# Performance work log

Measured on AMD Instinct MI355X. Metric: run time of the kernel, lower is better.

Reference implementation:

```python
import jax, jax.numpy as jnp
import numpy as np

B, L, F, H, N_HASHES = 2, 2048, 1024, 16, 4
HD = F // H  # head_dim = 64


def setup_inputs() -> dict:
    key = jax.random.key(0)
    ks = jax.random.split(key, 8)
    s = 0.02
    return {
        "x": jax.random.normal(ks[0], (B, L, F), jnp.float32),
        "Wqk": jax.random.normal(ks[1], (F, 2 * F), jnp.float32) * s,
        "bqk": jnp.zeros((2 * F,), jnp.float32),
        "Wv": jax.random.normal(ks[2], (F, F), jnp.float32) * s,
        "bv": jnp.zeros((F,), jnp.float32),
        "Wo": jax.random.normal(ks[3], (F, F), jnp.float32) * s,
        "bo": jnp.zeros((F,), jnp.float32),
        "R": jax.random.normal(ks[4], (H, N_HASHES, HD), jnp.float32) * s,
    }


def reference(x, Wqk, bqk, Wv, bv, Wo, bo, R):
    b, l, f = x.shape
    h, _, hd = R.shape

    qk = x @ Wqk + bqk                      # [B,L,2F]
    q, k = jnp.split(qk, 2, axis=-1)
    v = x @ Wv + bv                         # [B,L,F]

    def to_heads(t):
        return t.reshape(b, l, h, hd).transpose(0, 2, 1, 3)  # [B,H,L,D]

    q, k, v = to_heads(q), to_heads(k), to_heads(v)

    # LSH hashing of queries: argmax over [rotated, -rotated]
    rotated = jnp.einsum('bhld,hrd->bhlr', q, R)             # [B,H,L,n_hashes]
    buckets = jnp.argmax(jnp.concatenate([rotated, -rotated], axis=-1), axis=-1)  # [B,H,L]

    # Sort sequence positions by bucket id (per batch/head)
    idx = jnp.argsort(buckets, axis=-1)                      # [B,H,L]

    def gather_l(t):
        return jnp.take_along_axis(t, idx[..., None], axis=2)

    sq, sk, sv = gather_l(q), gather_l(k), gather_l(v)

    # Full dense attention over the sorted sequence
    scale = 1.0 / np.sqrt(hd).astype(np.float32)
    dots = jnp.einsum('bhqd,bhkd->bhqk', sq, sk) * scale     # [B,H,L,L]
    attn = jax.nn.softmax(dots, axis=-1)
    out = jnp.einsum('bhqk,bhkd->bhqd', attn, sv)            # [B,H,L,D]

    # Scatter back to original order
    restore = jnp.argsort(idx, axis=-1)
    out = jnp.take_along_axis(out, restore[..., None], axis=2)
    out = out.transpose(0, 2, 1, 3).reshape(b, l, f)
    return out @ Wo + bo
```

## Files before the change

kernel.cpp:

```cpp
#include <hip/hip_runtime.h>


#define B_ 2
#define L_ 2048
#define F_ 1024
#define H_ 16
#define D_ 64
#define M_ 4096

typedef unsigned short u16;
typedef unsigned int   u32;
typedef __bf16 bf16x8 __attribute__((ext_vector_type(8)));
typedef float  f32x4  __attribute__((ext_vector_type(4)));

__device__ __forceinline__ u16 f2bf(float f) {
    __bf16 h = (__bf16)f;
    return __builtin_bit_cast(u16, h);
}

__device__ __forceinline__ void glds16(const void* g, void* l) {
    __builtin_amdgcn_global_load_lds(
        (const __attribute__((address_space(1))) u32*)g,
        (__attribute__((address_space(3))) u32*)l, 16, 0, 0);
}

#define MFMA16(a, b, c) __builtin_amdgcn_mfma_f32_16x16x32_bf16(a, b, c, 0, 0, 0)

__global__ __launch_bounds__(256) void cast_x(const float* __restrict__ x, u16* __restrict__ xb) {
    int i0 = blockIdx.x * 256 + threadIdx.x;
    #pragma unroll
    for (int r = 0; r < 4; ++r) {
        int i = i0 + r * 262144;
        float4 v = ((const float4*)x)[i];
        ushort4 o; o.x = f2bf(v.x); o.y = f2bf(v.y); o.z = f2bf(v.z); o.w = f2bf(v.w);
        ((ushort4*)xb)[i] = o;
    }
}

__global__ __launch_bounds__(256) void tr_all(
    const float* __restrict__ Wqk, const float* __restrict__ Wv,
    const float* __restrict__ Wo, u16* __restrict__ Wt, u16* __restrict__ Wot)
{
    __shared__ float tile[32][33];
    const int z = blockIdx.z;
    const float* src; u16* dst; int N;
    if (z == 0)      { src = Wqk; dst = Wt;                       N = 2048; }
    else if (z == 1) { src = Wv;  dst = Wt + (size_t)2048 * 1024; N = 1024; }
    else             { src = Wo;  dst = Wot;                      N = 1024; }
    int n0 = blockIdx.x * 32, k0 = blockIdx.y * 32;
    if (n0 >= N) return;
    int tx = threadIdx.x & 31, ty = threadIdx.x >> 5;
    #pragma unroll
    for (int i = 0; i < 4; ++i) {
        int k = ty + i * 8;
        tile[k][tx] = src[(size_t)(k0 + k) * N + n0 + tx];
    }
    __syncthreads();
    #pragma unroll
    for (int i = 0; i < 4; ++i) {
        int n = ty + i * 8;
        dst[(size_t)(n0 + n) * 1024 + k0 + tx] = f2bf(tile[tx][n]);
    }
}

__device__ __forceinline__ void gemm_loop(
    const u16* __restrict__ A, const u16* __restrict__ Bt,
    size_t m0, size_t n0, u16* As, u16* Bs, int t, f32x4 acc[4][4])
{
    const int w = t >> 6, lane = t & 63, ml = lane & 15, quad = lane >> 4;
    const int mw = (w >> 1) * 64, nw = (w & 1) * 64;
    const int srow = (lane >> 2), schunk = (lane & 3) * 8;

    for (int k0 = 0; k0 < 1024; k0 += 32) {
        __syncthreads();
        #pragma unroll
        for (int i = 0; i < 2; ++i) {
            int row = w * 32 + i * 16 + srow;
            glds16(A  + (m0 + row) * 1024 + k0 + schunk, As + (w * 32 + i * 16) * 32);
            glds16(Bt + (n0 + row) * 1024 + k0 + schunk, Bs + (w * 32 + i * 16) * 32);
        }
        __syncthreads();
        bf16x8 af[4], bf_[4];
        #pragma unroll
        for (int mt = 0; mt < 4; ++mt)
            af[mt] = *(const bf16x8*)(As + (mw + mt * 16 + ml) * 32 + quad * 8);
        #pragma unroll
        for (int nt = 0; nt < 4; ++nt)
            bf_[nt] = *(const bf16x8*)(Bs + (nw + nt * 16 + ml) * 32 + quad * 8);
        #pragma unroll
        for (int mt = 0; mt < 4; ++mt)
            #pragma unroll
            for (int nt = 0; nt < 4; ++nt)
                acc[mt][nt] = MFMA16(af[mt], bf_[nt], acc[mt][nt]);
    }
}

__global__ __launch_bounds__(256) void qkv_gemm(
    const u16* __restrict__ xb, const u16* __restrict__ Wt,
    const float* __restrict__ bqk, const float* __restrict__ bv,
    u16* __restrict__ Qb, u16* __restrict__ Kb, u16* __restrict__ Vt)
{
    __shared__ __align__(16) u16 As[128 * 32];
    __shared__ __align__(16) u16 Bs[128 * 32];
    const int t = threadIdx.x;
    const size_t m0 = blockIdx.y * 128, n0 = blockIdx.x * 128;
    f32x4 acc[4][4] = {};
    gemm_loop(xb, Wt, m0, n0, As, Bs, t, acc);

    const int w = t >> 6, lane = t & 63, ml = lane & 15, quad = lane >> 4;
    const int mw = (w >> 1) * 64, nw = (w & 1) * 64;
    const int seg = (int)(n0 >> 10);

    #pragma unroll
    for (int mt = 0; mt < 4; ++mt) {
        #pragma unroll
        for (int nt = 0; nt < 4; ++nt) {
            f32x4 a = acc[mt][nt];
            int c = (int)n0 + nw + nt * 16 + ml;
            int mbase = (int)m0 + mw + mt * 16 + quad * 4;
            if (seg == 2) {
                int cv = c - 2048, h = cv >> 6, d = cv & 63;
                float bias = bv[cv];
                int bb = mbase >> 11, l0 = mbase & (L_ - 1);
                ushort4 pk;
                pk.x = f2bf(a[0] + bias); pk.y = f2bf(a[1] + bias);
                pk.z = f2bf(a[2] + bias); pk.w = f2bf(a[3] + bias);
                *(ushort4*)&Vt[(((size_t)(bb * H_ + h)) * D_ + d) * L_ + l0] = pk;
            } else {
                float bias = bqk[c];
                float sc = (seg == 0) ? 0.125f : 1.0f;
                u16* dst = (seg == 0) ? Qb : Kb;
                int cc = c & 1023, h = cc >> 6, d = cc & 63;
                #pragma unroll
                for (int reg = 0; reg < 4; ++reg) {
                    int m = mbase + reg, bb = m >> 11, l = m & (L_ - 1);
                    dst[(((size_t)(bb * H_ + h)) * L_ + l) * D_ + d] = f2bf((a[reg] + bias) * sc);
                }
            }
        }
    }
}

__global__ __launch_bounds__(256) void out_gemm(
    const u16* __restrict__ Ob, const u16* __restrict__ Wot,
    const float* __restrict__ bo, float* __restrict__ out)
{
    __shared__ __align__(16) u16 As[128 * 32];
    __shared__ __align__(16) u16 Bs[128 * 32];
    const int t = threadIdx.x;
    const size_t m0 = blockIdx.y * 128, n0 = blockIdx.x * 128;
    f32x4 acc[4][4] = {};
    gemm_loop(Ob, Wot, m0, n0, As, Bs, t, acc);

    const int w = t >> 6, lane = t & 63, ml = lane & 15, quad = lane >> 4;
    const int mw = (w >> 1) * 64, nw = (w & 1) * 64;
    #pragma unroll
    for (int mt = 0; mt < 4; ++mt)
        #pragma unroll
        for (int nt = 0; nt < 4; ++nt) {
            int c = (int)n0 + nw + nt * 16 + ml;
            int mbase = (int)m0 + mw + mt * 16 + quad * 4;
            float bias = bo[c];
            #pragma unroll
            for (int reg = 0; reg < 4; ++reg)
                out[(size_t)(mbase + reg) * F_ + c] = acc[mt][nt][reg] + bias;
        }
}

__device__ __forceinline__ bf16x8 frag(const u16* base, int row, int chunk) {
    return *(const bf16x8*)(base + row * 64 + ((chunk ^ (row & 7)) << 3));
}

__global__ __launch_bounds__(256) void attn_mfma(
    const u16* __restrict__ Qb, const u16* __restrict__ Kb,
    const u16* __restrict__ Vt, u16* __restrict__ Ob)
{
    __shared__ __align__(16) u16 Qs[128 * 64];
    __shared__ __align__(16) u16 Ks[64 * 64];
    __shared__ __align__(16) u16 Vs[64 * 64];
    __shared__ __align__(16) float Sw[4][32 * 68];
    __shared__ float Ls[4][32];

    const int t = threadIdx.x, w = t >> 6, lane = t & 63;
    const int ml = lane & 15, quad = lane >> 4;
    const int srow8 = lane >> 3, sch = lane & 7;
    const int qt = blockIdx.x, h = blockIdx.y, b = blockIdx.z;
    const size_t hoff = ((size_t)(b * H_ + h)) * L_ * D_;
    const u16* Qg = Qb + hoff + (size_t)qt * 128 * 64;
    const u16* Kg = Kb + hoff;
    const u16* Vg = Vt + hoff;

    #pragma unroll
    for (int i = 0; i < 4; ++i) {
        int row = w * 32 + i * 8 + srow8;
        int ch = sch ^ (row & 7);
        glds16(Qg + row * 64 + ch * 8, Qs + (w * 32 + i * 8) * 64);
    }
    __syncthreads();
    bf16x8 aq[2][2];
    #pragma unroll
    for (int m2 = 0; m2 < 2; ++m2)
        #pragma unroll
        for (int k2 = 0; k2 < 2; ++k2)
            aq[m2][k2] = frag(Qs, w * 32 + m2 * 16 + ml, k2 * 4 + quad);

    float psum[2] = {0.f, 0.f};
    f32x4 oacc[2][4] = {};
    float* Swp = Sw[w];

    for (int kt = 0; kt < 32; ++kt) {
        __syncthreads();
        #pragma unroll
        for (int i = 0; i < 2; ++i) {
            int row = w * 16 + i * 8 + srow8;
            int ch = sch ^ (row & 7);
            glds16(Kg + (size_t)(kt * 64 + row) * 64 + ch * 8, Ks + (w * 16 + i * 8) * 64);
            glds16(Vg + (size_t)row * L_ + kt * 64 + ch * 8,   Vs + (w * 16 + i * 8) * 64);
        }
        __syncthreads();

        f32x4 sacc[2][4] = {};
        #pragma unroll
        for (int k2 = 0; k2 < 2; ++k2) {
            bf16x8 bk[4];
            #pragma unroll
            for (int nt = 0; nt < 4; ++nt)
                bk[nt] = frag(Ks, nt * 16 + ml, k2 * 4 + quad);
            #pragma unroll
            for (int m2 = 0; m2 < 2; ++m2)
                #pragma unroll
                for (int nt = 0; nt < 4; ++nt)
                    sacc[m2][nt] = MFMA16(aq[m2][k2], bk[nt], sacc[m2][nt]);
        }

        #pragma unroll
        for (int m2 = 0; m2 < 2; ++m2)
            #pragma unroll
            for (int nt = 0; nt < 4; ++nt)
                #pragma unroll
                for (int r = 0; r < 4; ++r) {
                    int row = m2 * 16 + quad * 4 + r, col = nt * 16 + ml;
                    Swp[row * 68 + col] = __expf(sacc[m2][nt][r]);
                }

        #pragma unroll
        for (int k2 = 0; k2 < 2; ++k2) {
            bf16x8 bv8[4];
            #pragma unroll
            for (int nt = 0; nt < 4; ++nt)
                bv8[nt] = frag(Vs, nt * 16 + ml, k2 * 4 + quad);
            #pragma unroll
            for (int m2 = 0; m2 < 2; ++m2) {
                const float* pp = Swp + (m2 * 16 + ml) * 68 + (k2 * 4 + quad) * 8;
                f32x4 p0 = *(const f32x4*)pp;
                f32x4 p1 = *(const f32x4*)(pp + 4);
                psum[m2] += (p0[0] + p0[1] + p0[2] + p0[3]) +
                            (p1[0] + p1[1] + p1[2] + p1[3]);
                bf16x8 ap;
                ap[0] = (__bf16)p0[0]; ap[1] = (__bf16)p0[1];
                ap[2] = (__bf16)p0[2]; ap[3] = (__bf16)p0[3];
                ap[4] = (__bf16)p1[0]; ap[5] = (__bf16)p1[1];
                ap[6] = (__bf16)p1[2]; ap[7] = (__bf16)p1[3];
                #pragma unroll
                for (int nt = 0; nt < 4; ++nt)
                    oacc[m2][nt] = MFMA16(ap, bv8[nt], oacc[m2][nt]);
            }
        }
    }

    #pragma unroll
    for (int m2 = 0; m2 < 2; ++m2) {
        psum[m2] += __shfl_xor(psum[m2], 16);
        psum[m2] += __shfl_xor(psum[m2], 32);
    }
    if (quad == 0) { Ls[w][ml] = psum[0]; Ls[w][16 + ml] = psum[1]; }

    #pragma unroll
    for (int m2 = 0; m2 < 2; ++m2)
        #pragma unroll
        for (int r = 0; r < 4; ++r) {
            float il = 1.0f / Ls[w][m2 * 16 + quad * 4 + r];
            int row = b * L_ + qt * 128 + w * 32 + m2 * 16 + quad * 4 + r;
            #pragma unroll
            for (int nt = 0; nt < 4; ++nt) {
                int c = h * 64 + nt * 16 + ml;
                Ob[(size_t)row * F_ + c] = f2bf(oacc[m2][nt][r] * il);
            }
        }
}

extern "C" void kernel_launch(void* const* d_in, const int* in_sizes, int n_in,
                              void* d_out, int out_size, void* d_ws, size_t ws_size,
                              hipStream_t stream)
{
    const float* x   = (const float*)d_in[0];
    const float* Wqk = (const float*)d_in[1];
    const float* bqk = (const float*)d_in[2];
    const float* Wv  = (const float*)d_in[3];
    const float* bv  = (const float*)d_in[4];
    const float* Wo  = (const float*)d_in[5];
    const float* bo  = (const float*)d_in[6];
    (void)in_sizes; (void)n_in; (void)out_size; (void)ws_size;
    float* out = (float*)d_out;

    u16* w16 = (u16*)d_ws;
    u16* xb  = w16;
    u16* Wt  = xb  + 4194304;
    u16* Wot = Wt  + 3145728;
    u16* Qb  = Wot + 1048576;
    u16* Kb  = Qb  + 4194304;
    u16* Vtw = Kb  + 4194304;
    u16* Ob  = Vtw + 4194304;

    cast_x<<<1024, 256, 0, stream>>>(x, xb);
    tr_all<<<dim3(64, 32, 3), 256, 0, stream>>>(Wqk, Wv, Wo, Wt, Wot);
    qkv_gemm<<<dim3(24, 32), 256, 0, stream>>>(xb, Wt, bqk, bv, Qb, Kb, Vtw);
    attn_mfma<<<dim3(16, 16, 2), 256, 0, stream>>>(Qb, Kb, Vtw, Ob);
    out_gemm<<<dim3(8, 32), 256, 0, stream>>>(Ob, Wot, bo, out);
}
```

Before: 219.3 us.

## Drop LDS staging in attention; compute transposed scores in registers

The attention kernel stops staging Q, K and V tiles and exp-scores in shared memory. Each wave now loads its MFMA fragments straight from global memory and computes S^T (K as the A operand), so the exp'd probabilities already sit in the register layout needed for the P·V MFMA. This removes the LDS round-trip and all block-level barriers. The cost is that each wave re-reads K and V from global/L2 on its own, with narrow 8-byte loads for V, and the launch is flattened to 1D with a 2-blocks-per-CU occupancy hint.

```diff
diff --git a/kernel.cpp b/kernel.cpp
--- a/kernel.cpp
+++ b/kernel.cpp
@@ -167,105 +167,74 @@
         }
 }
 
-__device__ __forceinline__ bf16x8 frag(const u16* base, int row, int chunk) {
-    return *(const bf16x8*)(base + row * 64 + ((chunk ^ (row & 7)) << 3));
-}
-
-__global__ __launch_bounds__(256) void attn_mfma(
+__global__ __launch_bounds__(256, 2) void attn_mfma(
     const u16* __restrict__ Qb, const u16* __restrict__ Kb,
     const u16* __restrict__ Vt, u16* __restrict__ Ob)
 {
-    __shared__ __align__(16) u16 Qs[128 * 64];
-    __shared__ __align__(16) u16 Ks[64 * 64];
-    __shared__ __align__(16) u16 Vs[64 * 64];
-    __shared__ __align__(16) float Sw[4][32 * 68];
-    __shared__ float Ls[4][32];
-
     const int t = threadIdx.x, w = t >> 6, lane = t & 63;
     const int ml = lane & 15, quad = lane >> 4;
-    const int srow8 = lane >> 3, sch = lane & 7;
-    const int qt = blockIdx.x, h = blockIdx.y, b = blockIdx.z;
+    const int blk = blockIdx.x;
+    const int qt4 = blk & 15, bh = blk >> 4;
+    const int b = bh >> 4, h = bh & 15;
+    const int qbase = qt4 * 128 + w * 32;
     const size_t hoff = ((size_t)(b * H_ + h)) * L_ * D_;
-    const u16* Qg = Qb + hoff + (size_t)qt * 128 * 64;
+    const u16* Qg = Qb + hoff;
     const u16* Kg = Kb + hoff;
     const u16* Vg = Vt + hoff;
 
-    #pragma unroll
-    for (int i = 0; i < 4; ++i) {
-        int row = w * 32 + i * 8 + srow8;
-        int ch = sch ^ (row & 7);
-        glds16(Qg + row * 64 + ch * 8, Qs + (w * 32 + i * 8) * 64);
-    }
-    __syncthreads();
-    bf16x8 aq[2][2];
+    bf16x8 qf[2][2];
     #pragma unroll
     for (int m2 = 0; m2 < 2; ++m2)
         #pragma unroll
         for (int k2 = 0; k2 < 2; ++k2)
-            aq[m2][k2] = frag(Qs, w * 32 + m2 * 16 + ml, k2 * 4 + quad);
-
+            qf[m2][k2] = *(const bf16x8*)(Qg + (size_t)(qbase + m2 * 16 + ml) * 64 + k2 * 32 + quad * 8);
+
+    f32x4 oacc[2][4] = {};
     float psum[2] = {0.f, 0.f};
-    f32x4 oacc[2][4] = {};
-    float* Swp = Sw[w];
 
     for (int kt = 0; kt < 32; ++kt) {
-        __syncthreads();
-        #pragma unroll
-        for (int i = 0; i < 2; ++i) {
-            int row = w * 16 + i * 8 + srow8;
-            int ch = sch ^ (row & 7);
-            glds16(Kg + (size_t)(kt * 64 + row) * 64 + ch * 8, Ks + (w * 16 + i * 8) * 64);
-            glds16(Vg + (size_t)row * L_ + kt * 64 + ch * 8,   Vs + (w * 16 + i * 8) * 64);
-        }
-        __syncthreads();
+        const u16* Kt = Kg + (size_t)kt * 64 * 64;
+
+        bf16x8 kf[4][2];
+        #pragma unroll
+        for (int t4 = 0; t4 < 4; ++t4)
+            #pragma unroll
+            for (int k2 = 0; k2 < 2; ++k2)
+                kf[t4][k2] = *(const bf16x8*)(Kt + (size_t)(t4 * 16 + ml) * 64 + k2 * 32 + quad * 8);
 
         f32x4 sacc[2][4] = {};
         #pragma unroll
-        for (int k2 = 0; k2 < 2; ++k2) {
-            bf16x8 bk[4];
-            #pragma unroll
-            for (int nt = 0; nt < 4; ++nt)
-                bk[nt] = frag(Ks, nt * 16 + ml, k2 * 4 + quad);
-            #pragma unroll
-            for (int m2 = 0; m2 < 2; ++m2)
-                #pragma unroll
-                for (int nt = 0; nt < 4; ++nt)
-                    sacc[m2][nt] = MFMA16(aq[m2][k2], bk[nt], sacc[m2][nt]);
-        }
-
+        for (int k2 = 0; k2 < 2; ++k2)
+            #pragma unroll
+            for (int t4 = 0; t4 < 4; ++t4)
+                #pragma unroll
+                for (int m2 = 0; m2 < 2; ++m2)
+                    sacc[m2][t4] = MFMA16(kf[t4][k2], qf[m2][k2], sacc[m2][t4]);
+
+        bf16x8 ap[2][2];
         #pragma unroll
         for (int m2 = 0; m2 < 2; ++m2)
             #pragma unroll
-            for (int nt = 0; nt < 4; ++nt)
+            for (int t4 = 0; t4 < 4; ++t4)
                 #pragma unroll
                 for (int r = 0; r < 4; ++r) {
-                    int row = m2 * 16 + quad * 4 + r, col = nt * 16 + ml;
-                    Swp[row * 68 + col] = __expf(sacc[m2][nt][r]);
+                    float p = __expf(sacc[m2][t4][r]);
+                    psum[m2] += p;
+                    ap[m2][t4 >> 1][(t4 & 1) * 4 + r] = (__bf16)p;
                 }
 
         #pragma unroll
-        for (int k2 = 0; k2 < 2; ++k2) {
-            bf16x8 bv8[4];
-            #pragma unroll
-            for (int nt = 0; nt < 4; ++nt)
-                bv8[nt] = frag(Vs, nt * 16 + ml, k2 * 4 + quad);
-            #pragma unroll
-            for (int m2 = 0; m2 < 2; ++m2) {
-                const float* pp = Swp + (m2 * 16 + ml) * 68 + (k2 * 4 + quad) * 8;
-                f32x4 p0 = *(const f32x4*)pp;
-                f32x4 p1 = *(const f32x4*)(pp + 4);
-                psum[m2] += (p0[0] + p0[1] + p0[2] + p0[3]) +
-                            (p1[0] + p1[1] + p1[2] + p1[3]);
-                bf16x8 ap;
-                ap[0] = (__bf16)p0[0]; ap[1] = (__bf16)p0[1];
-                ap[2] = (__bf16)p0[2]; ap[3] = (__bf16)p0[3];
-                ap[4] = (__bf16)p1[0]; ap[5] = (__bf16)p1[1];
-                ap[6] = (__bf16)p1[2]; ap[7] = (__bf16)p1[3];
-                #pragma unroll
-                for (int nt = 0; nt < 4; ++nt)
-                    oacc[m2][nt] = MFMA16(ap, bv8[nt], oacc[m2][nt]);
+        for (int tp = 0; tp < 2; ++tp)
+            #pragma unroll
+            for (int dt = 0; dt < 4; ++dt) {
+                const u16* vp = Vg + (size_t)(dt * 16 + ml) * L_ + kt * 64 + tp * 32 + quad * 4;
+                bf16x8 vf;
+                *(ushort4*)&vf       = *(const ushort4*)vp;
+                *(((ushort4*)&vf)+1) = *(const ushort4*)(vp + 16);
+                #pragma unroll
+                for (int m2 = 0; m2 < 2; ++m2)
+                    oacc[m2][dt] = MFMA16(ap[m2][tp], vf, oacc[m2][dt]);
             }
-        }
     }
 
     #pragma unroll
@@ -273,18 +242,18 @@
         psum[m2] += __shfl_xor(psum[m2], 16);
         psum[m2] += __shfl_xor(psum[m2], 32);
     }
-    if (quad == 0) { Ls[w][ml] = psum[0]; Ls[w][16 + ml] = psum[1]; }
 
     #pragma unroll
     for (int m2 = 0; m2 < 2; ++m2)
         #pragma unroll
         for (int r = 0; r < 4; ++r) {
-            float il = 1.0f / Ls[w][m2 * 16 + quad * 4 + r];
-            int row = b * L_ + qt * 128 + w * 32 + m2 * 16 + quad * 4 + r;
-            #pragma unroll
-            for (int nt = 0; nt < 4; ++nt) {
-                int c = h * 64 + nt * 16 + ml;
-                Ob[(size_t)row * F_ + c] = f2bf(oacc[m2][nt][r] * il);
+            float s = __shfl(psum[m2], quad * 4 + r);
+            float il = 1.0f / s;
+            int row = b * L_ + qbase + m2 * 16 + quad * 4 + r;
+            #pragma unroll
+            for (int dt = 0; dt < 4; ++dt) {
+                int c = h * 64 + dt * 16 + ml;
+                Ob[(size_t)row * F_ + c] = f2bf(oacc[m2][dt][r] * il);
             }
         }
 }
@@ -315,6 +284,6 @@
     cast_x<<<1024, 256, 0, stream>>>(x, xb);
     tr_all<<<dim3(64, 32, 3), 256, 0, stream>>>(Wqk, Wv, Wo, Wt, Wot);
     qkv_gemm<<<dim3(24, 32), 256, 0, stream>>>(xb, Wt, bqk, bv, Qb, Kb, Vtw);
-    attn_mfma<<<dim3(16, 16, 2), 256, 0, stream>>>(Qb, Kb, Vtw, Ob);
+    attn_mfma<<<512, 256, 0, stream>>>(Qb, Kb, Vtw, Ob);
     out_gemm<<<dim3(8, 32), 256, 0, stream>>>(Ob, Wot, bo, out);
 }
```

Result: slower. 319.1 us (+45.5%).
